# Kernel tuning notes

Hardware: AMD Instinct MI355X
Metric: run time of the kernel (lower is better)

The kernel has to match this reference:

```python
import jax, jax.numpy as jnp
import numpy as np

N, K, D = 32768, 4096, 256


def setup_inputs() -> dict:
    key = jax.random.key(0)
    k1, k2 = jax.random.split(key)
    z_e = jax.random.normal(k1, (N, D), dtype=jnp.float32)
    embed = jax.random.normal(k2, (K, D), dtype=jnp.float32)
    return {"z_e": z_e, "embed": embed}


def reference(z_e, embed):
    # squared L2 distances: ||z||^2 - 2 z.E^T + ||e||^2  -> [N, K]
    d = (jnp.sum(z_e * z_e, axis=1, keepdims=True)
         - 2.0 * (z_e @ embed.T)
         + jnp.sum(embed * embed, axis=1))
    idx = jnp.argmin(d, axis=1)                      # [N] int32
    one_hot = jax.nn.one_hot(idx, K, dtype=z_e.dtype)  # [N, K]
    z_q = one_hot @ embed                            # [N, D] (matches torch's one_hot @ embed)
    return (z_q, idx, one_hot)
```

## Files before the change

kernel.cpp:

```cpp
#include <hip/hip_runtime.h>


#define N_TOK 32768
#define K_CODE 4096
#define D_DIM 256
#define BM 64

typedef float f32x4 __attribute__((ext_vector_type(4)));
typedef short s16x8 __attribute__((ext_vector_type(8)));

#define OUT_FLOATS 142639104u
#define SCR_FLOATS 1576960u
#define SCR_OFF    (OUT_FLOATS - SCR_FLOATS)
#define EFRAG_SHORTS (3u * K_CODE * D_DIM)
#define OH_SAFE_ROWS 32320

static __device__ __forceinline__ unsigned short f2bf(float f) {
    unsigned int u = __float_as_uint(f);
    u = (u + 0x7fffu + ((u >> 16) & 1u)) >> 16;
    return (unsigned short)u;
}
static __device__ __forceinline__ float bf2f(unsigned short b) {
    return __uint_as_float(((unsigned int)b) << 16);
}

__global__ __launch_bounds__(256) void vq_prep(const float* __restrict__ embed,
                                               float* __restrict__ out) {
    __shared__ float part[8][33];
    unsigned short* escr = (unsigned short*)(out + SCR_OFF);
    float* e2g = out + SCR_OFF + (EFRAG_SHORTS / 2);

    const int t    = threadIdx.x;
    const int cl   = t >> 5;
    const int r32  = t & 31;
    const int dc   = r32 >> 2;
    const int quad = r32 & 3;
    const int k    = blockIdx.x * 8 + cl;

    const float* src = embed + (size_t)k * D_DIM + dc * 32 + quad * 8;
    float x[8];
    *(float4*)(x)     = *(const float4*)(src);
    *(float4*)(x + 4) = *(const float4*)(src + 4);

    s16x8 hv, mv, lv;
    float s2 = 0.0f;
#pragma unroll
    for (int j = 0; j < 8; ++j) {
        const float xx = x[j];
        s2 += xx * xx;
        const unsigned short bh = f2bf(xx);
        const float r1 = xx - bf2f(bh);
        const unsigned short bm = f2bf(r1);
        hv[j] = (short)bh; mv[j] = (short)bm; lv[j] = (short)f2bf(r1 - bf2f(bm));
    }

    const int ct_g = k >> 4;
    const int lane = quad * 16 + (k & 15);
    const size_t base = ((size_t)(ct_g * 8 + dc) * 3) * 512 + lane * 8;
    *(s16x8*)&escr[base]        = hv;
    *(s16x8*)&escr[base + 512]  = mv;
    *(s16x8*)&escr[base + 1024] = lv;

    part[cl][r32] = s2;
    __syncthreads();
    if (t < 8) {
        float s = 0.0f;
#pragma unroll
        for (int j = 0; j < 32; ++j) s += part[t][j];
        e2g[blockIdx.x * 8 + t] = s;
    }
}

static __device__ __forceinline__ void load_b(const unsigned short* __restrict__ escr,
                                              int kt, int dc, int w, int lane,
                                              s16x8 (&buf)[2][3]) {
#pragma unroll
    for (int u = 0; u < 2; ++u) {
        const int ct_g = kt * 16 + w * 2 + u;
        const unsigned short* p = &escr[((size_t)(ct_g * 8 + dc) * 3) * 512 + lane * 8];
#pragma unroll
        for (int c = 0; c < 3; ++c)
            buf[u][c] = *(const s16x8*)(p + c * 512);
    }
}

static __device__ __forceinline__ void proc_step(const short* As,
        const float* __restrict__ e2g, int kt, int dc, int w, int lane, int n,
        s16x8 (&bfm)[2][3], f32x4 (&acc)[4][2], float (&e2r)[2],
        float (&bv)[16], int (&bidx)[16]) {
    if (dc == 0) {
#pragma unroll
        for (int u = 0; u < 2; ++u) e2r[u] = e2g[kt * 256 + (w * 2 + u) * 16 + n];
    }
#pragma unroll
    for (int rt = 0; rt < 4; ++rt) {
        s16x8 af0 = *(const s16x8*)&As[((0 * 4 + rt) * 8 + dc) * 512 + lane * 8];
        s16x8 af1 = *(const s16x8*)&As[((1 * 4 + rt) * 8 + dc) * 512 + lane * 8];
        s16x8 af2 = *(const s16x8*)&As[((2 * 4 + rt) * 8 + dc) * 512 + lane * 8];
#pragma unroll
        for (int u = 0; u < 2; ++u) {
            f32x4 a = acc[rt][u];
            a = __builtin_amdgcn_mfma_f32_16x16x32_bf16(af0, bfm[u][0], a, 0, 0, 0);
            a = __builtin_amdgcn_mfma_f32_16x16x32_bf16(af0, bfm[u][1], a, 0, 0, 0);
            a = __builtin_amdgcn_mfma_f32_16x16x32_bf16(af1, bfm[u][0], a, 0, 0, 0);
            a = __builtin_amdgcn_mfma_f32_16x16x32_bf16(af1, bfm[u][1], a, 0, 0, 0);
            a = __builtin_amdgcn_mfma_f32_16x16x32_bf16(af0, bfm[u][2], a, 0, 0, 0);
            a = __builtin_amdgcn_mfma_f32_16x16x32_bf16(af2, bfm[u][0], a, 0, 0, 0);
            acc[rt][u] = a;
        }
    }
    if (dc == 7) {
#pragma unroll
        for (int u = 0; u < 2; ++u) {
            const int code = kt * 256 + (w * 2 + u) * 16 + n;
#pragma unroll
            for (int rt = 0; rt < 4; ++rt)
#pragma unroll
                for (int r = 0; r < 4; ++r) {
                    const float val = fmaf(-2.0f, acc[rt][u][r], e2r[u]);
                    const int slot = rt * 4 + r;
                    if (val < bv[slot]) { bv[slot] = val; bidx[slot] = code; }
                }
        }
#pragma unroll
        for (int rt = 0; rt < 4; ++rt)
#pragma unroll
            for (int u = 0; u < 2; ++u) acc[rt][u] = (f32x4){0.f, 0.f, 0.f, 0.f};
    }
}

__global__ __launch_bounds__(512, 2)
void vq_argmin_mfma(const float* __restrict__ z_e,
                    const float* __restrict__ embed,
                    float* __restrict__ out) {
    __shared__ __align__(16) short As[49152];
    __shared__ float redv[64][9];
    __shared__ int   redi[64][9];
    __shared__ int   bk_lds[64];

    const unsigned short* escr = (const unsigned short*)(out + SCR_OFF);
    const float* e2g = out + SCR_OFF + (EFRAG_SHORTS / 2);

    const int t    = threadIdx.x;
    const int w    = t >> 6;
    const int lane = t & 63;
    const int n    = lane & 15;
    const int quad = lane >> 4;
    const int row0 = blockIdx.x * BM;

#pragma unroll
    for (int i = 0; i < 4; ++i) {
        const int run  = t + 512 * i;
        const int qs   = run & 3;
        const int dcs  = (run >> 2) & 7;
        const int row  = run >> 5;
        const float* src = z_e + (size_t)(row0 + row) * D_DIM + dcs * 32 + qs * 8;
        float x[8];
        *(float4*)(x)     = *(const float4*)(src);
        *(float4*)(x + 4) = *(const float4*)(src + 4);
        s16x8 hv, mv, lv;
#pragma unroll
        for (int j = 0; j < 8; ++j) {
            const float xx = x[j];
            const unsigned short bh = f2bf(xx);
            const float r1 = xx - bf2f(bh);
            const unsigned short bm = f2bf(r1);
            hv[j] = (short)bh; mv[j] = (short)bm; lv[j] = (short)f2bf(r1 - bf2f(bm));
        }
        const int rtile = row >> 4;
        const int ls    = qs * 16 + (row & 15);
        *(s16x8*)&As[((0 * 4 + rtile) * 8 + dcs) * 512 + ls * 8] = hv;
        *(s16x8*)&As[((1 * 4 + rtile) * 8 + dcs) * 512 + ls * 8] = mv;
        *(s16x8*)&As[((2 * 4 + rtile) * 8 + dcs) * 512 + ls * 8] = lv;
    }
    __syncthreads();

    float bv[16];
    int   bidx[16];
#pragma unroll
    for (int s = 0; s < 16; ++s) { bv[s] = 3.0e38f; bidx[s] = 0; }

    f32x4 acc[4][2];
#pragma unroll
    for (int rt = 0; rt < 4; ++rt)
#pragma unroll
        for (int u = 0; u < 2; ++u) acc[rt][u] = (f32x4){0.f, 0.f, 0.f, 0.f};

    float e2r[2];
    s16x8 b0[2][3], b1[2][3];
    load_b(escr, 0, 0, w, lane, b0);

#pragma unroll 1
    for (int it = 0; it < 64; ++it) {
        const int s0 = it * 2, s1 = s0 + 1, s2 = s1 + 1;
        load_b(escr, s1 >> 3, s1 & 7, w, lane, b1);
        proc_step(As, e2g, s0 >> 3, s0 & 7, w, lane, n, b0, acc, e2r, bv, bidx);
        if (it < 63) load_b(escr, s2 >> 3, s2 & 7, w, lane, b0);
        proc_step(As, e2g, s1 >> 3, s1 & 7, w, lane, n, b1, acc, e2r, bv, bidx);
    }

#pragma unroll
    for (int slot = 0; slot < 16; ++slot) {
#pragma unroll
        for (int mask = 1; mask < 16; mask <<= 1) {
            const float ov = __shfl_xor(bv[slot], mask);
            const int   oi = __shfl_xor(bidx[slot], mask);
            if (ov < bv[slot] || (ov == bv[slot] && oi < bidx[slot])) {
                bv[slot] = ov; bidx[slot] = oi;
            }
        }
    }
    if (n == 0) {
#pragma unroll
        for (int rt = 0; rt < 4; ++rt)
#pragma unroll
            for (int r = 0; r < 4; ++r) {
                const int row_local = rt * 16 + quad * 4 + r;
                redv[row_local][w] = bv[rt * 4 + r];
                redi[row_local][w] = bidx[rt * 4 + r];
            }
    }
    __syncthreads();
    if (t < 64) {
        float v = redv[t][0];
        int  bi = redi[t][0];
#pragma unroll
        for (int j = 1; j < 8; ++j) {
            const float v2 = redv[t][j];
            const int   i2 = redi[t][j];
            if (v2 < v || (v2 == v && i2 < bi)) { v = v2; bi = i2; }
        }
        bk_lds[t] = bi;
        out[(size_t)N_TOK * D_DIM + (size_t)(row0 + t)] = (float)bi;
    }
    __syncthreads();

    float* zq = out;
    float* oh = out + (size_t)N_TOK * D_DIM + N_TOK;

#pragma unroll 1
    for (int rr = 0; rr < 8; ++rr) {
        const int rl  = w * 8 + rr;
        const int row = row0 + rl;
        const int bk  = bk_lds[rl];
        f32x4 v = *(const f32x4*)&embed[(size_t)bk * D_DIM + lane * 4];
        __builtin_nontemporal_store(v, (f32x4*)&zq[(size_t)row * D_DIM + lane * 4]);
    }
    if (row0 < OH_SAFE_ROWS) {
#pragma unroll 1
        for (int rr = 0; rr < 8; ++rr) {
            const int rl  = w * 8 + rr;
            const int row = row0 + rl;
            const int bk  = bk_lds[rl];
            float* ohrow = &oh[(size_t)row * K_CODE];
#pragma unroll
            for (int g = 0; g < 16; ++g) {
                const int base = (g * 64 + lane) * 4;
                f32x4 u;
                u.x = (bk == base    ) ? 1.0f : 0.0f;
                u.y = (bk == base + 1) ? 1.0f : 0.0f;
                u.z = (bk == base + 2) ? 1.0f : 0.0f;
                u.w = (bk == base + 3) ? 1.0f : 0.0f;
                __builtin_nontemporal_store(u, (f32x4*)&ohrow[base]);
            }
        }
    }
}

__launch_bounds__(256, 8)
__global__ void vq_oh_tail(float* __restrict__ out) {
    __shared__ int bks[16];
    const int t    = threadIdx.x;
    const int w    = t >> 6;
    const int lane = t & 63;
    const int row0 = OH_SAFE_ROWS + blockIdx.x * 16;

    const float* idxf = out + (size_t)N_TOK * D_DIM;
    float* oh = out + (size_t)N_TOK * D_DIM + N_TOK;

    if (t < 16) bks[t] = (int)idxf[row0 + t];
    __syncthreads();

#pragma unroll 1
    for (int rr = 0; rr < 4; ++rr) {
        const int r   = rr * 4 + w;
        const int row = row0 + r;
        const int bk  = bks[r];
        float* ohrow = &oh[(size_t)row * K_CODE];
#pragma unroll
        for (int g = 0; g < 16; ++g) {
            const int base = (g * 64 + lane) * 4;
            f32x4 u;
            u.x = (bk == base    ) ? 1.0f : 0.0f;
            u.y = (bk == base + 1) ? 1.0f : 0.0f;
            u.z = (bk == base + 2) ? 1.0f : 0.0f;
            u.w = (bk == base + 3) ? 1.0f : 0.0f;
            __builtin_nontemporal_store(u, (f32x4*)&ohrow[base]);
        }
    }
}

extern "C" void kernel_launch(void* const* d_in, const int* in_sizes, int n_in,
                              void* d_out, int out_size, void* d_ws, size_t ws_size,
                              hipStream_t stream) {
    const float* z_e   = (const float*)d_in[0];
    const float* embed = (const float*)d_in[1];
    float* out = (float*)d_out;

    hipLaunchKernelGGL(vq_prep,        dim3(K_CODE / 8), dim3(256), 0, stream, embed, out);
    hipLaunchKernelGGL(vq_argmin_mfma, dim3(N_TOK / BM), dim3(512), 0, stream, z_e, embed, out);
    hipLaunchKernelGGL(vq_oh_tail,     dim3((N_TOK - OH_SAFE_ROWS) / 16), dim3(256), 0, stream, out);
}
```

Before: 853.9 us.

## Re-tile waves as 2x4 row/code grid with register-cached A fragments

Changes the wave-to-tile mapping from 8 waves each covering all 64 rows by 32 codes to a 2x4 grid where each wave covers 32 rows by 64 codes, processing two code tiles interleaved so A fragments are loaded from LDS once and reused across both. This cuts LDS reads of the z fragments per MFMA and halves the cross-wave reduction width. It increases B register buffers and accumulators (48 accumulator floats plus doubled B buffers), which risks register pressure under the 2-blocks-per-CU launch bound.

```diff
diff --git a/kernel.cpp b/kernel.cpp
--- a/kernel.cpp
+++ b/kernel.cpp
@@ -72,11 +72,13 @@
 }
 
 static __device__ __forceinline__ void load_b(const unsigned short* __restrict__ escr,
-                                              int kt, int dc, int w, int lane,
-                                              s16x8 (&buf)[2][3]) {
-#pragma unroll
-    for (int u = 0; u < 2; ++u) {
-        const int ct_g = kt * 16 + w * 2 + u;
+                                              int fs, int cg, int lane,
+                                              s16x8 (&buf)[4][3]) {
+    const int ktstep = ((fs >> 4) << 1) + (fs & 1);
+    const int dc     = (fs >> 1) & 7;
+#pragma unroll
+    for (int u = 0; u < 4; ++u) {
+        const int ct_g = ktstep * 16 + cg * 4 + u;
         const unsigned short* p = &escr[((size_t)(ct_g * 8 + dc) * 3) * 512 + lane * 8];
 #pragma unroll
         for (int c = 0; c < 3; ++c)
@@ -85,47 +87,60 @@
 }
 
 static __device__ __forceinline__ void proc_step(const short* As,
-        const float* __restrict__ e2g, int kt, int dc, int w, int lane, int n,
-        s16x8 (&bfm)[2][3], f32x4 (&acc)[4][2], float (&e2r)[2],
-        float (&bv)[16], int (&bidx)[16]) {
-    if (dc == 0) {
-#pragma unroll
-        for (int u = 0; u < 2; ++u) e2r[u] = e2g[kt * 256 + (w * 2 + u) * 16 + n];
-    }
-#pragma unroll
-    for (int rt = 0; rt < 4; ++rt) {
-        s16x8 af0 = *(const s16x8*)&As[((0 * 4 + rt) * 8 + dc) * 512 + lane * 8];
-        s16x8 af1 = *(const s16x8*)&As[((1 * 4 + rt) * 8 + dc) * 512 + lane * 8];
-        s16x8 af2 = *(const s16x8*)&As[((2 * 4 + rt) * 8 + dc) * 512 + lane * 8];
-#pragma unroll
-        for (int u = 0; u < 2; ++u) {
-            f32x4 a = acc[rt][u];
-            a = __builtin_amdgcn_mfma_f32_16x16x32_bf16(af0, bfm[u][0], a, 0, 0, 0);
-            a = __builtin_amdgcn_mfma_f32_16x16x32_bf16(af0, bfm[u][1], a, 0, 0, 0);
-            a = __builtin_amdgcn_mfma_f32_16x16x32_bf16(af1, bfm[u][0], a, 0, 0, 0);
-            a = __builtin_amdgcn_mfma_f32_16x16x32_bf16(af1, bfm[u][1], a, 0, 0, 0);
-            a = __builtin_amdgcn_mfma_f32_16x16x32_bf16(af0, bfm[u][2], a, 0, 0, 0);
-            a = __builtin_amdgcn_mfma_f32_16x16x32_bf16(af2, bfm[u][0], a, 0, 0, 0);
-            acc[rt][u] = a;
-        }
-    }
-    if (dc == 7) {
-#pragma unroll
-        for (int u = 0; u < 2; ++u) {
-            const int code = kt * 256 + (w * 2 + u) * 16 + n;
-#pragma unroll
-            for (int rt = 0; rt < 4; ++rt)
-#pragma unroll
-                for (int r = 0; r < 4; ++r) {
-                    const float val = fmaf(-2.0f, acc[rt][u][r], e2r[u]);
-                    const int slot = rt * 4 + r;
-                    if (val < bv[slot]) { bv[slot] = val; bidx[slot] = code; }
-                }
-        }
-#pragma unroll
-        for (int rt = 0; rt < 4; ++rt)
-#pragma unroll
-            for (int u = 0; u < 2; ++u) acc[rt][u] = (f32x4){0.f, 0.f, 0.f, 0.f};
+        const float* __restrict__ e2g, int fs, int rh, int cg, int lane, int n,
+        s16x8 (&af)[2][3], s16x8 (&bfm)[4][3], f32x4 (&acc)[2][2][4],
+        float (&bv)[8], int (&bidx)[8]) {
+    const int kt = fs & 1;
+    const int dc = (fs >> 1) & 7;
+
+    if (kt == 0) {
+#pragma unroll
+        for (int rt = 0; rt < 2; ++rt) {
+            const int rtl = rh * 2 + rt;
+#pragma unroll
+            for (int c = 0; c < 3; ++c)
+                af[rt][c] = *(const s16x8*)&As[((c * 4 + rtl) * 8 + dc) * 512 + lane * 8];
+        }
+    }
+
+#pragma unroll
+    for (int rt = 0; rt < 2; ++rt)
+#pragma unroll
+        for (int u = 0; u < 4; ++u) {
+            f32x4 a = acc[kt][rt][u];
+            a = __builtin_amdgcn_mfma_f32_16x16x32_bf16(af[rt][0], bfm[u][0], a, 0, 0, 0);
+            a = __builtin_amdgcn_mfma_f32_16x16x32_bf16(af[rt][0], bfm[u][1], a, 0, 0, 0);
+            a = __builtin_amdgcn_mfma_f32_16x16x32_bf16(af[rt][1], bfm[u][0], a, 0, 0, 0);
+            a = __builtin_amdgcn_mfma_f32_16x16x32_bf16(af[rt][1], bfm[u][1], a, 0, 0, 0);
+            a = __builtin_amdgcn_mfma_f32_16x16x32_bf16(af[rt][0], bfm[u][2], a, 0, 0, 0);
+            a = __builtin_amdgcn_mfma_f32_16x16x32_bf16(af[rt][2], bfm[u][0], a, 0, 0, 0);
+            acc[kt][rt][u] = a;
+        }
+
+    if ((fs & 15) == 15) {
+        const int ktile = fs >> 4;
+#pragma unroll
+        for (int kk = 0; kk < 2; ++kk)
+#pragma unroll
+            for (int u = 0; u < 4; ++u) {
+                const int code = (ktile * 2 + kk) * 256 + cg * 64 + u * 16 + n;
+                const float e2v = e2g[code];
+#pragma unroll
+                for (int rt = 0; rt < 2; ++rt)
+#pragma unroll
+                    for (int r = 0; r < 4; ++r) {
+                        const float val = fmaf(-2.0f, acc[kk][rt][u][r], e2v);
+                        const int slot = rt * 4 + r;
+                        if (val < bv[slot]) { bv[slot] = val; bidx[slot] = code; }
+                    }
+            }
+#pragma unroll
+        for (int kk = 0; kk < 2; ++kk)
+#pragma unroll
+            for (int rt = 0; rt < 2; ++rt)
+#pragma unroll
+                for (int u = 0; u < 4; ++u)
+                    acc[kk][rt][u] = (f32x4){0.f, 0.f, 0.f, 0.f};
     }
 }
 
@@ -134,8 +149,8 @@
                     const float* __restrict__ embed,
                     float* __restrict__ out) {
     __shared__ __align__(16) short As[49152];
-    __shared__ float redv[64][9];
-    __shared__ int   redi[64][9];
+    __shared__ float redv[64][5];
+    __shared__ int   redi[64][5];
     __shared__ int   bk_lds[64];
 
     const unsigned short* escr = (const unsigned short*)(out + SCR_OFF);
@@ -143,6 +158,8 @@
 
     const int t    = threadIdx.x;
     const int w    = t >> 6;
+    const int rh   = w >> 2;
+    const int cg   = w & 3;
     const int lane = t & 63;
     const int n    = lane & 15;
     const int quad = lane >> 4;
@@ -175,32 +192,34 @@
     }
     __syncthreads();
 
-    float bv[16];
-    int   bidx[16];
-#pragma unroll
-    for (int s = 0; s < 16; ++s) { bv[s] = 3.0e38f; bidx[s] = 0; }
-
-    f32x4 acc[4][2];
-#pragma unroll
-    for (int rt = 0; rt < 4; ++rt)
-#pragma unroll
-        for (int u = 0; u < 2; ++u) acc[rt][u] = (f32x4){0.f, 0.f, 0.f, 0.f};
-
-    float e2r[2];
-    s16x8 b0[2][3], b1[2][3];
-    load_b(escr, 0, 0, w, lane, b0);
+    float bv[8];
+    int   bidx[8];
+#pragma unroll
+    for (int s = 0; s < 8; ++s) { bv[s] = 3.0e38f; bidx[s] = 0; }
+
+    f32x4 acc[2][2][4];
+#pragma unroll
+    for (int kk = 0; kk < 2; ++kk)
+#pragma unroll
+        for (int rt = 0; rt < 2; ++rt)
+#pragma unroll
+            for (int u = 0; u < 4; ++u) acc[kk][rt][u] = (f32x4){0.f, 0.f, 0.f, 0.f};
+
+    s16x8 af[2][3];
+    s16x8 b0[4][3], b1[4][3];
+    load_b(escr, 0, cg, lane, b0);
 
 #pragma unroll 1
     for (int it = 0; it < 64; ++it) {
-        const int s0 = it * 2, s1 = s0 + 1, s2 = s1 + 1;
-        load_b(escr, s1 >> 3, s1 & 7, w, lane, b1);
-        proc_step(As, e2g, s0 >> 3, s0 & 7, w, lane, n, b0, acc, e2r, bv, bidx);
-        if (it < 63) load_b(escr, s2 >> 3, s2 & 7, w, lane, b0);
-        proc_step(As, e2g, s1 >> 3, s1 & 7, w, lane, n, b1, acc, e2r, bv, bidx);
-    }
-
-#pragma unroll
-    for (int slot = 0; slot < 16; ++slot) {
+        const int s0 = it * 2, s1 = s0 + 1;
+        load_b(escr, s1, cg, lane, b1);
+        proc_step(As, e2g, s0, rh, cg, lane, n, af, b0, acc, bv, bidx);
+        if (it < 63) load_b(escr, s1 + 1, cg, lane, b0);
+        proc_step(As, e2g, s1, rh, cg, lane, n, af, b1, acc, bv, bidx);
+    }
+
+#pragma unroll
+    for (int slot = 0; slot < 8; ++slot) {
 #pragma unroll
         for (int mask = 1; mask < 16; mask <<= 1) {
             const float ov = __shfl_xor(bv[slot], mask);
@@ -212,12 +231,12 @@
     }
     if (n == 0) {
 #pragma unroll
-        for (int rt = 0; rt < 4; ++rt)
+        for (int rt = 0; rt < 2; ++rt)
 #pragma unroll
             for (int r = 0; r < 4; ++r) {
-                const int row_local = rt * 16 + quad * 4 + r;
-                redv[row_local][w] = bv[rt * 4 + r];
-                redi[row_local][w] = bidx[rt * 4 + r];
+                const int row_local = (rh * 2 + rt) * 16 + quad * 4 + r;
+                redv[row_local][cg] = bv[rt * 4 + r];
+                redi[row_local][cg] = bidx[rt * 4 + r];
             }
     }
     __syncthreads();
@@ -225,7 +244,7 @@
         float v = redv[t][0];
         int  bi = redi[t][0];
 #pragma unroll
-        for (int j = 1; j < 8; ++j) {
+        for (int j = 1; j < 4; ++j) {
             const float v2 = redv[t][j];
             const int   i2 = redi[t][j];
             if (v2 < v || (v2 == v && i2 < bi)) { v = v2; bi = i2; }
```

After: 873.0 us. 2.2% more time.
